# Kernel tuning notes

Hardware: AMD Instinct MI355X
Metric: run time of the kernel (lower is better)

Reference implementation:

```python
import jax, jax.numpy as jnp
import numpy as np

B, T, D = 4, 8192, 1024
N_PROTO = 8


def setup_inputs() -> dict:
    key = jax.random.key(0)
    k1, k2, k3 = jax.random.split(key, 3)
    x = jax.random.normal(k1, (B, T, D), dtype=jnp.float32)
    # torch Linear kaiming-uniform scale ~ 1/sqrt(fan_in); keeps tanh unsaturated
    W = jax.random.normal(k2, (6, D), dtype=jnp.float32) * (1.0 / np.sqrt(D))
    prototypes = jax.random.normal(k3, (N_PROTO, 6), dtype=jnp.float32)
    hamming_scale = jnp.float32(0.1)
    return {"x": x, "W": W, "prototypes": prototypes, "hamming_scale": hamming_scale}


def reference(x, W, prototypes, hamming_scale):
    # q6_project: tanh(Linear(x)) then L2-normalize with clamp(min=1e-6)
    z = jnp.tanh(jnp.einsum('btd,kd->btk', x, W))            # (B,T,6)
    z = z / jnp.clip(jnp.linalg.norm(z, axis=-1, keepdims=True), 1e-6)
    # F.normalize(prototypes, dim=-1) with eps=1e-12
    p = prototypes / jnp.clip(jnp.linalg.norm(prototypes, axis=-1, keepdims=True), 1e-12)
    dot = jnp.einsum('btk,pk->btp', z, p)                    # (B,T,P)
    dist = (6.0 - dot * 6.0) * 0.5                            # Theorem-3 Hamming distance
    return jax.nn.softmax(-hamming_scale * dist, axis=-1)    # routing weights (B,T,P)
```

## Files before the change

kernel.cpp:

```cpp
#include <hip/hip_runtime.h>


#define DIM 1024
#define NK 6
#define NPROTO 8

__global__ __launch_bounds__(256, 2) void q6_fused_kernel(
    const float* __restrict__ x,
    const float* __restrict__ W,
    const float* __restrict__ protos,
    const float* __restrict__ hs_ptr,
    float* __restrict__ out,
    int n_tokens, int n_waves)
{
    const int lane = threadIdx.x & 63;
    const int wave_id = blockIdx.x * (blockDim.x >> 6) + (threadIdx.x >> 6);
    const int cbase = lane * 4;

    float4 wreg[NK][4];
#pragma unroll
    for (int k = 0; k < NK; ++k)
#pragma unroll
        for (int j = 0; j < 4; ++j)
            wreg[k][j] = *reinterpret_cast<const float4*>(&W[k * DIM + j * 256 + cbase]);

    const int pl = lane & 7;
    float p0 = protos[pl * 6 + 0], p1 = protos[pl * 6 + 1], p2 = protos[pl * 6 + 2];
    float p3 = protos[pl * 6 + 3], p4 = protos[pl * 6 + 4], p5 = protos[pl * 6 + 5];
    {
        float pn = sqrtf(p0*p0 + p1*p1 + p2*p2 + p3*p3 + p4*p4 + p5*p5);
        float inv = 1.0f / fmaxf(pn, 1e-12f);
        p0 *= inv; p1 *= inv; p2 *= inv; p3 *= inv; p4 *= inv; p5 *= inv;
    }
    const float hs = hs_ptr[0];

    for (int t = wave_id; t < n_tokens; t += n_waves) {
        const float* xt = x + (size_t)t * DIM;
        float acc0 = 0.f, acc1 = 0.f, acc2 = 0.f, acc3 = 0.f, acc4 = 0.f, acc5 = 0.f;
#pragma unroll
        for (int j = 0; j < 4; ++j) {
            float4 xv = *reinterpret_cast<const float4*>(&xt[j * 256 + cbase]);
            acc0 = fmaf(xv.x, wreg[0][j].x, acc0); acc0 = fmaf(xv.y, wreg[0][j].y, acc0);
            acc0 = fmaf(xv.z, wreg[0][j].z, acc0); acc0 = fmaf(xv.w, wreg[0][j].w, acc0);
            acc1 = fmaf(xv.x, wreg[1][j].x, acc1); acc1 = fmaf(xv.y, wreg[1][j].y, acc1);
            acc1 = fmaf(xv.z, wreg[1][j].z, acc1); acc1 = fmaf(xv.w, wreg[1][j].w, acc1);
            acc2 = fmaf(xv.x, wreg[2][j].x, acc2); acc2 = fmaf(xv.y, wreg[2][j].y, acc2);
            acc2 = fmaf(xv.z, wreg[2][j].z, acc2); acc2 = fmaf(xv.w, wreg[2][j].w, acc2);
            acc3 = fmaf(xv.x, wreg[3][j].x, acc3); acc3 = fmaf(xv.y, wreg[3][j].y, acc3);
            acc3 = fmaf(xv.z, wreg[3][j].z, acc3); acc3 = fmaf(xv.w, wreg[3][j].w, acc3);
            acc4 = fmaf(xv.x, wreg[4][j].x, acc4); acc4 = fmaf(xv.y, wreg[4][j].y, acc4);
            acc4 = fmaf(xv.z, wreg[4][j].z, acc4); acc4 = fmaf(xv.w, wreg[4][j].w, acc4);
            acc5 = fmaf(xv.x, wreg[5][j].x, acc5); acc5 = fmaf(xv.y, wreg[5][j].y, acc5);
            acc5 = fmaf(xv.z, wreg[5][j].z, acc5); acc5 = fmaf(xv.w, wreg[5][j].w, acc5);
        }
#pragma unroll
        for (int off = 32; off >= 1; off >>= 1) {
            acc0 += __shfl_xor(acc0, off, 64);
            acc1 += __shfl_xor(acc1, off, 64);
            acc2 += __shfl_xor(acc2, off, 64);
            acc3 += __shfl_xor(acc3, off, 64);
            acc4 += __shfl_xor(acc4, off, 64);
            acc5 += __shfl_xor(acc5, off, 64);
        }
        if (lane < NPROTO) {
            float z[NK];
            float a_in[NK] = {acc0, acc1, acc2, acc3, acc4, acc5};
#pragma unroll
            for (int k = 0; k < NK; ++k) {
                float a = a_in[k];
                float e = __expf(-2.0f * fabsf(a));
                float th = (1.0f - e) / (1.0f + e);
                z[k] = copysignf(th, a);
            }
            float nrm = sqrtf(z[0]*z[0] + z[1]*z[1] + z[2]*z[2] +
                              z[3]*z[3] + z[4]*z[4] + z[5]*z[5]);
            float inv = 1.0f / fmaxf(nrm, 1e-6f);
            float dot = (z[0]*p0 + z[1]*p1 + z[2]*p2 + z[3]*p3 + z[4]*p4 + z[5]*p5) * inv;
            float logit = -hs * (6.0f - dot * 6.0f) * 0.5f;
            float m = logit;
            m = fmaxf(m, __shfl_xor(m, 1, 64));
            m = fmaxf(m, __shfl_xor(m, 2, 64));
            m = fmaxf(m, __shfl_xor(m, 4, 64));
            float e = __expf(logit - m);
            float s = e;
            s += __shfl_xor(s, 1, 64);
            s += __shfl_xor(s, 2, 64);
            s += __shfl_xor(s, 4, 64);
            out[(size_t)t * NPROTO + lane] = e / s;
        }
    }
}

extern "C" void kernel_launch(void* const* d_in, const int* in_sizes, int n_in,
                              void* d_out, int out_size, void* d_ws, size_t ws_size,
                              hipStream_t stream) {
    const float* x      = (const float*)d_in[0];
    const float* W      = (const float*)d_in[1];
    const float* protos = (const float*)d_in[2];
    const float* hs     = (const float*)d_in[3];
    float* out = (float*)d_out;

    const int n_tokens = in_sizes[0] / DIM;
    const int blocks = 2048;
    const int threads = 256;
    const int n_waves = blocks * (threads / 64);

    q6_fused_kernel<<<blocks, threads, 0, stream>>>(
        x, W, protos, hs, out, n_tokens, n_waves);
}
```

Before: 194.9 us.

## Process four tokens per wave with transpose-style shuffle reduction

Each wave now loads four tokens' rows at once and computes their six dot products together. The cross-lane reduction uses a butterfly that swaps partial sums between lane halves, so the four tokens finish in separate 16-lane groups with fewer total shuffles. Tanh, normalisation and softmax then run in parallel for the four tokens. This is meant to raise memory-level parallelism and amortise shuffle cost, at the price of more registers under launch bounds of 256 threads with 2 blocks per unit. It also assumes the token count is a multiple of four.

```diff
diff --git a/kernel.cpp b/kernel.cpp
--- a/kernel.cpp
+++ b/kernel.cpp
@@ -4,6 +4,7 @@
 #define DIM 1024
 #define NK 6
 #define NPROTO 8
+#define TPI 4
 
 __global__ __launch_bounds__(256, 2) void q6_fused_kernel(
     const float* __restrict__ x,
@@ -25,57 +26,91 @@
             wreg[k][j] = *reinterpret_cast<const float4*>(&W[k * DIM + j * 256 + cbase]);
 
     const int pl = lane & 7;
-    float p0 = protos[pl * 6 + 0], p1 = protos[pl * 6 + 1], p2 = protos[pl * 6 + 2];
-    float p3 = protos[pl * 6 + 3], p4 = protos[pl * 6 + 4], p5 = protos[pl * 6 + 5];
+    float p[NK];
+#pragma unroll
+    for (int k = 0; k < NK; ++k) p[k] = protos[pl * NK + k];
     {
-        float pn = sqrtf(p0*p0 + p1*p1 + p2*p2 + p3*p3 + p4*p4 + p5*p5);
+        float pn = sqrtf(p[0]*p[0] + p[1]*p[1] + p[2]*p[2] + p[3]*p[3] + p[4]*p[4] + p[5]*p[5]);
         float inv = 1.0f / fmaxf(pn, 1e-12f);
-        p0 *= inv; p1 *= inv; p2 *= inv; p3 *= inv; p4 *= inv; p5 *= inv;
+#pragma unroll
+        for (int k = 0; k < NK; ++k) p[k] *= inv;
     }
     const float hs = hs_ptr[0];
 
-    for (int t = wave_id; t < n_tokens; t += n_waves) {
-        const float* xt = x + (size_t)t * DIM;
-        float acc0 = 0.f, acc1 = 0.f, acc2 = 0.f, acc3 = 0.f, acc4 = 0.f, acc5 = 0.f;
+    const bool hi5 = (lane & 32) != 0;
+    const bool hi4 = (lane & 16) != 0;
+    const int tloc = lane >> 4;
+    const int pidx = lane & 15;
+
+    for (int tb = wave_id * TPI; tb < n_tokens; tb += n_waves * TPI) {
+        float4 xv[TPI][4];
 #pragma unroll
-        for (int j = 0; j < 4; ++j) {
-            float4 xv = *reinterpret_cast<const float4*>(&xt[j * 256 + cbase]);
-            acc0 = fmaf(xv.x, wreg[0][j].x, acc0); acc0 = fmaf(xv.y, wreg[0][j].y, acc0);
-            acc0 = fmaf(xv.z, wreg[0][j].z, acc0); acc0 = fmaf(xv.w, wreg[0][j].w, acc0);
-            acc1 = fmaf(xv.x, wreg[1][j].x, acc1); acc1 = fmaf(xv.y, wreg[1][j].y, acc1);
-            acc1 = fmaf(xv.z, wreg[1][j].z, acc1); acc1 = fmaf(xv.w, wreg[1][j].w, acc1);
-            acc2 = fmaf(xv.x, wreg[2][j].x, acc2); acc2 = fmaf(xv.y, wreg[2][j].y, acc2);
-            acc2 = fmaf(xv.z, wreg[2][j].z, acc2); acc2 = fmaf(xv.w, wreg[2][j].w, acc2);
-            acc3 = fmaf(xv.x, wreg[3][j].x, acc3); acc3 = fmaf(xv.y, wreg[3][j].y, acc3);
-            acc3 = fmaf(xv.z, wreg[3][j].z, acc3); acc3 = fmaf(xv.w, wreg[3][j].w, acc3);
-            acc4 = fmaf(xv.x, wreg[4][j].x, acc4); acc4 = fmaf(xv.y, wreg[4][j].y, acc4);
-            acc4 = fmaf(xv.z, wreg[4][j].z, acc4); acc4 = fmaf(xv.w, wreg[4][j].w, acc4);
-            acc5 = fmaf(xv.x, wreg[5][j].x, acc5); acc5 = fmaf(xv.y, wreg[5][j].y, acc5);
-            acc5 = fmaf(xv.z, wreg[5][j].z, acc5); acc5 = fmaf(xv.w, wreg[5][j].w, acc5);
+        for (int t = 0; t < TPI; ++t) {
+            const float* xt = x + (size_t)(tb + t) * DIM;
+#pragma unroll
+            for (int j = 0; j < 4; ++j)
+                xv[t][j] = *reinterpret_cast<const float4*>(&xt[j * 256 + cbase]);
         }
+
+        float acc[TPI][NK];
 #pragma unroll
-        for (int off = 32; off >= 1; off >>= 1) {
-            acc0 += __shfl_xor(acc0, off, 64);
-            acc1 += __shfl_xor(acc1, off, 64);
-            acc2 += __shfl_xor(acc2, off, 64);
-            acc3 += __shfl_xor(acc3, off, 64);
-            acc4 += __shfl_xor(acc4, off, 64);
-            acc5 += __shfl_xor(acc5, off, 64);
-        }
-        if (lane < NPROTO) {
-            float z[NK];
-            float a_in[NK] = {acc0, acc1, acc2, acc3, acc4, acc5};
+        for (int t = 0; t < TPI; ++t)
+#pragma unroll
+            for (int k = 0; k < NK; ++k) acc[t][k] = 0.0f;
+#pragma unroll
+        for (int t = 0; t < TPI; ++t)
+#pragma unroll
+            for (int j = 0; j < 4; ++j) {
+                const float4 xvj = xv[t][j];
+#pragma unroll
+                for (int k = 0; k < NK; ++k) {
+                    float a = acc[t][k];
+                    a = fmaf(xvj.x, wreg[k][j].x, a);
+                    a = fmaf(xvj.y, wreg[k][j].y, a);
+                    a = fmaf(xvj.z, wreg[k][j].z, a);
+                    a = fmaf(xvj.w, wreg[k][j].w, a);
+                    acc[t][k] = a;
+                }
+            }
+
+        float r[2][NK];
+#pragma unroll
+        for (int tp = 0; tp < 2; ++tp)
 #pragma unroll
             for (int k = 0; k < NK; ++k) {
-                float a = a_in[k];
+                float send = hi5 ? acc[tp][k]     : acc[2 + tp][k];
+                float keep = hi5 ? acc[2 + tp][k] : acc[tp][k];
+                r[tp][k] = keep + __shfl_xor(send, 32, 64);
+            }
+
+        float z[NK];
+#pragma unroll
+        for (int k = 0; k < NK; ++k) {
+            float send = hi4 ? r[0][k] : r[1][k];
+            float keep = hi4 ? r[1][k] : r[0][k];
+            z[k] = keep + __shfl_xor(send, 16, 64);
+        }
+
+#pragma unroll
+        for (int off = 8; off >= 1; off >>= 1)
+#pragma unroll
+            for (int k = 0; k < NK; ++k)
+                z[k] += __shfl_xor(z[k], off, 64);
+
+        if (pidx < NPROTO) {
+            float zz[NK];
+            float nrm2 = 0.0f;
+#pragma unroll
+            for (int k = 0; k < NK; ++k) {
+                float a = z[k];
                 float e = __expf(-2.0f * fabsf(a));
                 float th = (1.0f - e) / (1.0f + e);
-                z[k] = copysignf(th, a);
+                zz[k] = copysignf(th, a);
+                nrm2 = fmaf(zz[k], zz[k], nrm2);
             }
-            float nrm = sqrtf(z[0]*z[0] + z[1]*z[1] + z[2]*z[2] +
-                              z[3]*z[3] + z[4]*z[4] + z[5]*z[5]);
-            float inv = 1.0f / fmaxf(nrm, 1e-6f);
-            float dot = (z[0]*p0 + z[1]*p1 + z[2]*p2 + z[3]*p3 + z[4]*p4 + z[5]*p5) * inv;
+            float inv = 1.0f / fmaxf(sqrtf(nrm2), 1e-6f);
+            float dot = (zz[0]*p[0] + zz[1]*p[1] + zz[2]*p[2] +
+                         zz[3]*p[3] + zz[4]*p[4] + zz[5]*p[5]) * inv;
             float logit = -hs * (6.0f - dot * 6.0f) * 0.5f;
             float m = logit;
             m = fmaxf(m, __shfl_xor(m, 1, 64));
@@ -86,7 +121,7 @@
             s += __shfl_xor(s, 1, 64);
             s += __shfl_xor(s, 2, 64);
             s += __shfl_xor(s, 4, 64);
-            out[(size_t)t * NPROTO + lane] = e / s;
+            out[(size_t)(tb + tloc) * NPROTO + pidx] = e / s;
         }
     }
 }
```

Result: no change. 192.1 us (-1.4%).
